# Kernel optimization log

Measured on AMD Instinct MI355X. Metric: run time of the kernel, lower is better.

The kernel has to match this reference:

```python
import math
import jax, jax.numpy as jnp
import numpy as np

B, S, D, H, HD, FF = 2, 2048, 2048, 16, 128, 5632
EPS = 1e-5


def rmsnorm(h, w):
    # LLaMA RMSNorm: x * rsqrt(mean(x^2) + eps) * weight
    return h * jax.lax.rsqrt(jnp.mean(h * h, axis=-1, keepdims=True) + EPS) * w


def cross_attn(q_in, kv_in, wq, wk, wv, wo):
    # start_pos = 0 and zero-init cache => keys/values are exactly the fresh xk/xv
    b, sq, _ = q_in.shape
    sk = kv_in.shape[1]
    q = (q_in @ wq.T).reshape(b, sq, H, HD)
    k = (kv_in @ wk.T).reshape(b, sk, H, HD)
    v = (kv_in @ wv.T).reshape(b, sk, H, HD)
    scores = jnp.einsum('bqhd,bkhd->bhqk', q, k) / math.sqrt(HD)
    p = jax.nn.softmax(scores.astype(jnp.float32), axis=-1).astype(q.dtype)
    o = jnp.einsum('bhqk,bkhd->bqhd', p, v).reshape(b, sq, H * HD)
    return o @ wo.T


def llama_output(h, residual_in, w1, w2, w3, norm_w):
    # SwiGLU FFN then post-residual RMSNorm (as in LLaMAOutput)
    ff = (jax.nn.silu(h @ w1.T) * (h @ w3.T)) @ w2.T
    return rmsnorm(ff + residual_in, norm_w)


def setup_inputs() -> dict:
    key = jax.random.key(0)
    ks = jax.random.split(key, 20)
    w = lambda k, shape: jax.random.normal(k, shape, jnp.float32) * 0.02
    return {
        'x': jax.random.normal(ks[0], (B, S, D), jnp.float32),
        'y': jax.random.normal(ks[1], (B, S, D), jnp.float32),
        'attn_norm_w': jnp.ones((D,), jnp.float32),
        'wq_x': w(ks[2], (D, D)), 'wk_x': w(ks[3], (D, D)),
        'wv_x': w(ks[4], (D, D)), 'wo_x': w(ks[5], (D, D)),
        'wq_y': w(ks[6], (D, D)), 'wk_y': w(ks[7], (D, D)),
        'wv_y': w(ks[8], (D, D)), 'wo_y': w(ks[9], (D, D)),
        'w1_x': w(ks[10], (FF, D)), 'w2_x': w(ks[11], (D, FF)), 'w3_x': w(ks[12], (FF, D)),
        'ffn_norm_x': jnp.ones((D,), jnp.float32),
        'w1_y': w(ks[13], (FF, D)), 'w2_y': w(ks[14], (D, FF)), 'w3_y': w(ks[15], (FF, D)),
        'ffn_norm_y': jnp.ones((D,), jnp.float32),
        'start_pos': 0,
    }


def reference(x, y, attn_norm_w,
              wq_x, wk_x, wv_x, wo_x,
              wq_y, wk_y, wv_y, wo_y,
              w1_x, w2_x, w3_x, ffn_norm_x,
              w1_y, w2_y, w3_y, ffn_norm_y,
              start_pos):
    del start_pos  # 0: cache slice [:, :0+S] equals fresh xk/xv
    xn = rmsnorm(x, attn_norm_w)
    yn = rmsnorm(y, attn_norm_w)
    out_x = cross_attn(xn, yn, wq_x, wk_x, wv_x, wo_x)
    out_y = cross_attn(yn, xn, wq_y, wk_y, wv_y, wo_y)
    return (llama_output(out_x, x, w1_x, w2_x, w3_x, ffn_norm_x),
            llama_output(out_y, y, w1_y, w2_y, w3_y, ffn_norm_y))
```

## Files before the change

### kernel.cpp

```cpp
#include <hip/hip_runtime.h>
#include <cstdio>
#include <cstdint>
#include <cstddef>

#define B_ 2
#define S_ 2048
#define D_ 2048
#define H_ 16
#define HD_ 128
#define FF_ 5632

typedef unsigned short u16;
typedef float f32x4 __attribute__((ext_vector_type(4)));
typedef __bf16 bf16x8 __attribute__((ext_vector_type(8)));
typedef short s16x8 __attribute__((ext_vector_type(8)));
typedef short s16x4 __attribute__((ext_vector_type(4)));

__device__ __forceinline__ u16 f2bf(float f) {
  unsigned u = __builtin_bit_cast(unsigned, f);
  u += 0x7fffu + ((u >> 16) & 1u);
  return (u16)(u >> 16);
}
__device__ __forceinline__ float bf2f(u16 h) {
  unsigned u = ((unsigned)h) << 16;
  return __builtin_bit_cast(float, u);
}

__device__ __forceinline__ void async_ld16(const void* g, void* l) {
  __builtin_amdgcn_global_load_lds(
      (__attribute__((address_space(1))) void*)(unsigned long long)g,
      (__attribute__((address_space(3))) void*)(unsigned)(unsigned long long)l,
      16, 0, 0);
}

__global__ __launch_bounds__(256) void k_cvt_bf16(
    const float* __restrict__ in, u16* __restrict__ out, int n8) {
  const int i = blockIdx.x * 256 + threadIdx.x;
  if (i >= n8) return;
  const float4* p = (const float4*)in + (size_t)i * 2;
  const float4 a = p[0], b = p[1];
  s16x8 o;
  o[0] = (short)f2bf(a.x); o[1] = (short)f2bf(a.y);
  o[2] = (short)f2bf(a.z); o[3] = (short)f2bf(a.w);
  o[4] = (short)f2bf(b.x); o[5] = (short)f2bf(b.y);
  o[6] = (short)f2bf(b.z); o[7] = (short)f2bf(b.w);
  *(s16x8*)(out + (size_t)i * 8) = o;
}

__global__ __launch_bounds__(256) void k_rmsnorm_bf16(
    const float* __restrict__ x, const float* __restrict__ w, u16* __restrict__ out) {
  const int row = blockIdx.x;
  const int t = threadIdx.x;
  const float* xr = x + (size_t)row * D_;
  const float4 a = ((const float4*)xr)[t];
  const float4 b = ((const float4*)xr)[t + 256];
  float ss = a.x * a.x + a.y * a.y + a.z * a.z + a.w * a.w +
             b.x * b.x + b.y * b.y + b.z * b.z + b.w * b.w;
#pragma unroll
  for (int off = 1; off < 64; off <<= 1) ss += __shfl_xor(ss, off);
  __shared__ float red[4];
  if ((t & 63) == 0) red[t >> 6] = ss;
  __syncthreads();
  const float scale =
      rsqrtf((red[0] + red[1] + red[2] + red[3]) * (1.0f / (float)D_) + 1e-5f);
  const float4 wa = ((const float4*)w)[t];
  const float4 wb = ((const float4*)w)[t + 256];
  u16* orow = out + (size_t)row * D_;
  s16x4 o0, o1;
  o0[0] = (short)f2bf(a.x * scale * wa.x);
  o0[1] = (short)f2bf(a.y * scale * wa.y);
  o0[2] = (short)f2bf(a.z * scale * wa.z);
  o0[3] = (short)f2bf(a.w * scale * wa.w);
  o1[0] = (short)f2bf(b.x * scale * wb.x);
  o1[1] = (short)f2bf(b.y * scale * wb.y);
  o1[2] = (short)f2bf(b.z * scale * wb.z);
  o1[3] = (short)f2bf(b.w * scale * wb.w);
  *(s16x4*)(orow + t * 4) = o0;
  *(s16x4*)(orow + (t + 256) * 4) = o1;
}

__global__ __launch_bounds__(256) void k_add_rmsnorm(
    const float* __restrict__ ff, const float* __restrict__ res,
    const float* __restrict__ w, float* __restrict__ out) {
  const int row = blockIdx.x;
  const int t = threadIdx.x;
  const float4 fa = ((const float4*)(ff + (size_t)row * D_))[t];
  const float4 fb = ((const float4*)(ff + (size_t)row * D_))[t + 256];
  const float4 ra = ((const float4*)(res + (size_t)row * D_))[t];
  const float4 rb = ((const float4*)(res + (size_t)row * D_))[t + 256];
  float4 ha, hb2;
  ha.x = fa.x + ra.x; ha.y = fa.y + ra.y; ha.z = fa.z + ra.z; ha.w = fa.w + ra.w;
  hb2.x = fb.x + rb.x; hb2.y = fb.y + rb.y; hb2.z = fb.z + rb.z; hb2.w = fb.w + rb.w;
  float ss = ha.x * ha.x + ha.y * ha.y + ha.z * ha.z + ha.w * ha.w +
             hb2.x * hb2.x + hb2.y * hb2.y + hb2.z * hb2.z + hb2.w * hb2.w;
#pragma unroll
  for (int off = 1; off < 64; off <<= 1) ss += __shfl_xor(ss, off);
  __shared__ float red[4];
  if ((t & 63) == 0) red[t >> 6] = ss;
  __syncthreads();
  const float scale =
      rsqrtf((red[0] + red[1] + red[2] + red[3]) * (1.0f / (float)D_) + 1e-5f);
  const float4 wa = ((const float4*)w)[t];
  const float4 wb = ((const float4*)w)[t + 256];
  float4 o0, o1;
  o0.x = ha.x * scale * wa.x; o0.y = ha.y * scale * wa.y;
  o0.z = ha.z * scale * wa.z; o0.w = ha.w * scale * wa.w;
  o1.x = hb2.x * scale * wb.x; o1.y = hb2.y * scale * wb.y;
  o1.z = hb2.z * scale * wb.z; o1.w = hb2.w * scale * wb.w;
  float* orow = out + (size_t)row * D_;
  ((float4*)orow)[t] = o0;
  ((float4*)orow)[t + 256] = o1;
}

__global__ __launch_bounds__(256) void k_silu_mul(
    const u16* __restrict__ gcat, u16* __restrict__ out) {
  const int idx = blockIdx.x * 256 + threadIdx.x;
  const int row = idx / 704;
  const int c = (idx - row * 704) * 8;
  const s16x8 gv = *(const s16x8*)(gcat + (size_t)row * 11264 + c);
  const s16x8 uv = *(const s16x8*)(gcat + (size_t)row * 11264 + 5632 + c);
  s16x8 ov;
#pragma unroll
  for (int j = 0; j < 8; j++) {
    float gf = bf2f((u16)gv[j]);
    float uf = bf2f((u16)uv[j]);
    float s = gf / (1.0f + __expf(-gf));
    ov[j] = (short)f2bf(s * uf);
  }
  *(s16x8*)(out + (size_t)row * 5632 + c) = ov;
}

template <int MODE>
__global__ __launch_bounds__(256, 2) void k_gemm_bt(
    const u16* __restrict__ A, const u16* __restrict__ Bm, void* __restrict__ Cp,
    u16* __restrict__ VT, int M, int N, int K, int ldc) {
  __shared__ __align__(16) u16 sA[128 * 32];
  __shared__ __align__(16) u16 sB[128 * 32];
  const int tid = threadIdx.x;
  const int lane = tid & 63;
  const int wave = tid >> 6;
  const int l15 = lane & 15;
  const int quad = lane >> 4;
  const int wm = (wave >> 1) * 64;
  const int wn = (wave & 1) * 64;
  const int bm = blockIdx.y * 128;
  const int bn = blockIdx.x * 128;

  const int sr = tid >> 2;
  const int sc = (tid & 3) * 8;
  const u16* pa = A + (size_t)(bm + sr) * K + sc;
  const u16* pb = Bm + (size_t)(bn + sr) * K + sc;
  u16* la = &sA[tid * 8];
  u16* lb = &sB[tid * 8];
  const size_t half = (size_t)64 * K;

  f32x4 acc[4][4] = {};
  const u16* ra = &sA[(wm + l15) * 32 + quad * 8];
  const u16* rb = &sB[(wn + l15) * 32 + quad * 8];

  for (int k0 = 0; k0 < K; k0 += 32) {
    async_ld16(pa, la);
    async_ld16(pa + half, la + 2048);
    async_ld16(pb, lb);
    async_ld16(pb + half, lb + 2048);
    pa += 32;
    pb += 32;
    __syncthreads();
    bf16x8 af[4], bfr[4];
#pragma unroll
    for (int i = 0; i < 4; i++) af[i] = *(const bf16x8*)(ra + i * 512);
#pragma unroll
    for (int j = 0; j < 4; j++) bfr[j] = *(const bf16x8*)(rb + j * 512);
#pragma unroll
    for (int i = 0; i < 4; i++)
#pragma unroll
      for (int j = 0; j < 4; j++)
        acc[i][j] = __builtin_amdgcn_mfma_f32_16x16x32_bf16(af[i], bfr[j],
                                                            acc[i][j], 0, 0, 0);
    __syncthreads();
  }

  if (MODE == 2 && bn >= 4096) {
#pragma unroll
    for (int i = 0; i < 4; i++)
#pragma unroll
      for (int j = 0; j < 4; j++) {
        const int row0 = bm + wm + i * 16 + quad * 4;
        const int cv = bn + wn + j * 16 + l15 - 4096;
        s16x4 o;
#pragma unroll
        for (int r = 0; r < 4; r++) o[r] = (short)f2bf(acc[i][j][r]);
        *(s16x4*)(VT + (size_t)cv * 4096 + row0) = o;
      }
    return;
  }
#pragma unroll
  for (int i = 0; i < 4; i++)
#pragma unroll
    for (int j = 0; j < 4; j++) {
      const int row0 = bm + wm + i * 16 + quad * 4;
      const int col = bn + wn + j * 16 + l15;
      if (MODE == 1) {
        float* C = (float*)Cp;
#pragma unroll
        for (int r = 0; r < 4; r++)
          C[(size_t)(row0 + r) * ldc + col] = acc[i][j][r];
      } else {
        u16* C = (u16*)Cp;
#pragma unroll
        for (int r = 0; r < 4; r++)
          C[(size_t)(row0 + r) * ldc + col] = f2bf(acc[i][j][r]);
      }
    }
}

__global__ __launch_bounds__(256) void k_flash(
    const u16* __restrict__ Qm, const u16* __restrict__ Km,
    const u16* __restrict__ VTm, u16* __restrict__ Om) {
  __shared__ __align__(16) u16 sK[32 * 136];
  __shared__ __align__(16) u16 sVT[128 * 40];
  __shared__ __align__(16) u16 sP[4][32 * 40];

  const int tid = threadIdx.x;
  const int lane = tid & 63;
  const int wave = tid >> 6;
  const int l15 = lane & 15;
  const int quad = lane >> 4;

  const int b = blockIdx.z;
  const int h = blockIdx.y;
  const int q0 = blockIdx.x * 128;
  const int LDQ = 6144;
  const size_t rowbase = (size_t)b * 2048;

  bf16x8 aq[2][4];
#pragma unroll
  for (int mi = 0; mi < 2; mi++) {
    const u16* qp = Qm + (rowbase + q0 + wave * 32 + mi * 16 + l15) * LDQ + h * 128;
#pragma unroll
    for (int c = 0; c < 4; c++)
      aq[mi][c] = *(const bf16x8*)(qp + c * 32 + quad * 8);
  }

  f32x4 o[2][8] = {};
  float l[2][4] = {};

  const int kr0 = tid >> 4;
  const int kc = (tid & 15) * 8;
  const int vhd = tid >> 2;
  const int vko = (tid & 3) * 8;

  const u16* Kbase = Km + rowbase * LDQ + h * 128;
  const u16* Vbase = VTm + (size_t)(h * 128) * 4096 + rowbase;

  const float rs = 0.08838834764831845f;

  for (int k0 = 0; k0 < S_; k0 += 32) {
    __syncthreads();
    {
      const s16x8 kv0 = *(const s16x8*)(Kbase + (size_t)(k0 + kr0) * LDQ + kc);
      const s16x8 kv1 = *(const s16x8*)(Kbase + (size_t)(k0 + kr0 + 16) * LDQ + kc);
      const s16x8 vv0 = *(const s16x8*)(Vbase + (size_t)vhd * 4096 + k0 + vko);
      const s16x8 vv1 = *(const s16x8*)(Vbase + (size_t)(vhd + 64) * 4096 + k0 + vko);
      *(s16x8*)(&sK[kr0 * 136 + kc]) = kv0;
      *(s16x8*)(&sK[(kr0 + 16) * 136 + kc]) = kv1;
      *(s16x8*)(&sVT[vhd * 40 + vko]) = vv0;
      *(s16x8*)(&sVT[(vhd + 64) * 40 + vko]) = vv1;
    }
    __syncthreads();

    bf16x8 bk[2][4];
#pragma unroll
    for (int nt = 0; nt < 2; nt++)
#pragma unroll
      for (int c = 0; c < 4; c++)
        bk[nt][c] = *(const bf16x8*)(&sK[(nt * 16 + l15) * 136 + c * 32 + quad * 8]);

#pragma unroll
    for (int mi = 0; mi < 2; mi++) {
      f32x4 s[2] = {};
#pragma unroll
      for (int nt = 0; nt < 2; nt++)
#pragma unroll
        for (int c = 0; c < 4; c++)
          s[nt] = __builtin_amdgcn_mfma_f32_16x16x32_bf16(aq[mi][c], bk[nt][c],
                                                          s[nt], 0, 0, 0);
#pragma unroll
      for (int nt = 0; nt < 2; nt++)
#pragma unroll
        for (int r = 0; r < 4; r++) {
          float pv = __expf(s[nt][r] * rs);
          l[mi][r] += pv;
          sP[wave][(mi * 16 + quad * 4 + r) * 40 + nt * 16 + l15] = f2bf(pv);
        }
    }

    bf16x8 ap[2];
#pragma unroll
    for (int mi = 0; mi < 2; mi++)
      ap[mi] = *(const bf16x8*)(&sP[wave][(mi * 16 + l15) * 40 + quad * 8]);
#pragma unroll
    for (int ht = 0; ht < 8; ht++) {
      bf16x8 bv = *(const bf16x8*)(&sVT[(ht * 16 + l15) * 40 + quad * 8]);
#pragma unroll
      for (int mi = 0; mi < 2; mi++)
        o[mi][ht] = __builtin_amdgcn_mfma_f32_16x16x32_bf16(ap[mi], bv,
                                                            o[mi][ht], 0, 0, 0);
    }
  }

#pragma unroll
  for (int mi = 0; mi < 2; mi++)
#pragma unroll
    for (int r = 0; r < 4; r++) {
      float s = l[mi][r];
      s += __shfl_xor(s, 1);
      s += __shfl_xor(s, 2);
      s += __shfl_xor(s, 4);
      s += __shfl_xor(s, 8);
      l[mi][r] = 1.0f / s;
    }
#pragma unroll
  for (int mi = 0; mi < 2; mi++)
#pragma unroll
    for (int r = 0; r < 4; r++) {
      const size_t ro =
          (rowbase + q0 + wave * 32 + mi * 16 + quad * 4 + r) * (size_t)D_ +
          (size_t)h * HD_;
      const float inv = l[mi][r];
#pragma unroll
      for (int ht = 0; ht < 8; ht++)
        Om[ro + ht * 16 + l15] = f2bf(o[mi][ht][r] * inv);
    }
}

extern "C" void kernel_launch(void* const* d_in, const int* in_sizes, int n_in,
                              void* d_out, int out_size, void* d_ws, size_t ws_size,
                              hipStream_t stream) {
  (void)in_sizes; (void)n_in; (void)out_size;

  const float* x = (const float*)d_in[0];
  const float* y = (const float*)d_in[1];
  const float* attn_norm_w = (const float*)d_in[2];
  const float* wq[2] = {(const float*)d_in[3], (const float*)d_in[7]};
  const float* wk[2] = {(const float*)d_in[4], (const float*)d_in[8]};
  const float* wv[2] = {(const float*)d_in[5], (const float*)d_in[9]};
  const float* wo[2] = {(const float*)d_in[6], (const float*)d_in[10]};
  const float* w1[2] = {(const float*)d_in[11], (const float*)d_in[15]};
  const float* w2[2] = {(const float*)d_in[12], (const float*)d_in[16]};
  const float* w3[2] = {(const float*)d_in[13], (const float*)d_in[17]};
  const float* fnw[2] = {(const float*)d_in[14], (const float*)d_in[18]};

  char* ws = (char*)d_ws;
  const size_t A0 = 0;
  const size_t A1 = 16777216;
  const size_t W_ = 33554432;
  const size_t Q1 = 79691776;
  const size_t Q2 = 130023424;
  const size_t V1 = 180355072;
  const size_t V2 = 197132288;
  const size_t GB = 213909504;
  const size_t NEED = 260046848;
  if (ws_size < NEED) {
    fprintf(stderr, "kernel_launch: ws too small: %zu < %zu\n", ws_size, NEED);
    return;
  }
  u16* xn = (u16*)(ws + A0);
  u16* yn = (u16*)(ws + A1);
  u16* wslot = (u16*)(ws + W_);
  u16* qkvA = (u16*)(ws + Q1);
  u16* qkvB = (u16*)(ws + Q2);
  u16* vtA = (u16*)(ws + V1);
  u16* vtB = (u16*)(ws + V2);
  u16* ao = (u16*)(ws + A0);
  u16* hbx = (u16*)(ws + A1);
  u16* hby = (u16*)(ws + V1);
  u16* gcat = (u16*)(ws + Q1);
  u16* gbuf = (u16*)(ws + GB);
  float* ff = (float*)(ws + Q1);

  const size_t WOFF = (size_t)2048 * 2048;

  k_rmsnorm_bf16<<<4096, 256, 0, stream>>>(x, attn_norm_w, xn);
  k_rmsnorm_bf16<<<4096, 256, 0, stream>>>(y, attn_norm_w, yn);

  const dim3 gqkv(48, 32);
  const dim3 gproj(16, 32);
  const dim3 gw13(88, 32);

  k_cvt_bf16<<<2048, 256, 0, stream>>>(wq[0], wslot, 524288);
  k_cvt_bf16<<<2048, 256, 0, stream>>>(wk[1], wslot + WOFF, 524288);
  k_cvt_bf16<<<2048, 256, 0, stream>>>(wv[1], wslot + 2 * WOFF, 524288);
  k_gemm_bt<2><<<gqkv, 256, 0, stream>>>(xn, wslot, qkvA, vtA, 4096, 6144, 2048, 6144);
  k_cvt_bf16<<<2048, 256, 0, stream>>>(wq[1], wslot, 524288);
  k_cvt_bf16<<<2048, 256, 0, stream>>>(wk[0], wslot + WOFF, 524288);
  k_cvt_bf16<<<2048, 256, 0, stream>>>(wv[0], wslot + 2 * WOFF, 524288);
  k_gemm_bt<2><<<gqkv, 256, 0, stream>>>(yn, wslot, qkvB, vtB, 4096, 6144, 2048, 6144);

  k_flash<<<dim3(16, 16, 2), 256, 0, stream>>>(qkvA, qkvB + 2048, vtB, ao);
  k_cvt_bf16<<<2048, 256, 0, stream>>>(wo[0], wslot, 524288);
  k_gemm_bt<0><<<gproj, 256, 0, stream>>>(ao, wslot, hbx, nullptr, 4096, 2048, 2048, 2048);

  k_flash<<<dim3(16, 16, 2), 256, 0, stream>>>(qkvB, qkvA + 2048, vtA, ao);
  k_cvt_bf16<<<2048, 256, 0, stream>>>(wo[1], wslot, 524288);
  k_gemm_bt<0><<<gproj, 256, 0, stream>>>(ao, wslot, hby, nullptr, 4096, 2048, 2048, 2048);

  const float* resid[2] = {x, y};
  float* outp[2] = {(float*)d_out, (float*)d_out + (size_t)8388608};
  u16* hb[2] = {hbx, hby};
  const size_t W13OFF = (size_t)FF_ * 2048;

  for (int s = 0; s < 2; s++) {
    k_cvt_bf16<<<5632, 256, 0, stream>>>(w1[s], wslot, 1441792);
    k_cvt_bf16<<<5632, 256, 0, stream>>>(w3[s], wslot + W13OFF, 1441792);
    k_gemm_bt<0><<<gw13, 256, 0, stream>>>(hb[s], wslot, gcat, nullptr, 4096, 11264, 2048, 11264);
    k_silu_mul<<<11264, 256, 0, stream>>>(gcat, gbuf);
    k_cvt_bf16<<<5632, 256, 0, stream>>>(w2[s], wslot, 1441792);
    k_gemm_bt<1><<<gproj, 256, 0, stream>>>(gbuf, wslot, ff, nullptr, 4096, 2048, 5632, 2048);
    k_add_rmsnorm<<<4096, 256, 0, stream>>>(ff, resid[s], fnw[s], outp[s]);
  }
}
```

Before: 1.772 ms.

## Add 256x256 double-buffered GEMM kernel for QKV and W1/W3 projections

Result: faster. 1.685 ms (-4.9%).

```diff
diff --git a/kernel.cpp b/kernel.cpp
--- a/kernel.cpp
+++ b/kernel.cpp
@@ -180,20 +180,6 @@
     __syncthreads();
   }
 
-  if (MODE == 2 && bn >= 4096) {
-#pragma unroll
-    for (int i = 0; i < 4; i++)
-#pragma unroll
-      for (int j = 0; j < 4; j++) {
-        const int row0 = bm + wm + i * 16 + quad * 4;
-        const int cv = bn + wn + j * 16 + l15 - 4096;
-        s16x4 o;
-#pragma unroll
-        for (int r = 0; r < 4; r++) o[r] = (short)f2bf(acc[i][j][r]);
-        *(s16x4*)(VT + (size_t)cv * 4096 + row0) = o;
-      }
-    return;
-  }
 #pragma unroll
   for (int i = 0; i < 4; i++)
 #pragma unroll
@@ -211,6 +197,119 @@
         for (int r = 0; r < 4; r++)
           C[(size_t)(row0 + r) * ldc + col] = f2bf(acc[i][j][r]);
       }
+    }
+  (void)VT;
+}
+
+template <int MODE>
+__global__ __launch_bounds__(512, 2) void k_gemm256(
+    const u16* __restrict__ A, const u16* __restrict__ Bm, void* __restrict__ Cp,
+    u16* __restrict__ VT, int M, int N, int K, int ldc) {
+  __shared__ __align__(16) char smem[131072];
+  (void)M; (void)N;
+  const int tid = threadIdx.x;
+  const int lane = tid & 63;
+  const int w = tid >> 6;
+  const int l15 = lane & 15;
+  const int quad = lane >> 4;
+  const int wr = w >> 2;
+  const int wc = w & 3;
+  const int bm = blockIdx.y * 256;
+  const int bn = blockIdx.x * 256;
+
+  const int srow = w * 8 + (lane >> 3);
+  const int scol = ((lane & 7) ^ ((lane >> 3) & 7)) * 8;
+  const int sloff = w * 1024 + lane * 16;
+  const u16* const pa = A + (size_t)(bm + srow) * K + scol;
+  const u16* const pb = Bm + (size_t)(bn + srow) * K + scol;
+  const size_t rs64 = (size_t)64 * K;
+
+  const int fxor = (l15 & 7) << 4;
+  const int c0 = (quad * 16) ^ fxor;
+  const int c1 = (64 + quad * 16) ^ fxor;
+  const int aRow = (wr * 128 + l15) * 128;
+  const int bRow = 32768 + (wc * 64 + l15) * 128;
+
+  f32x4 acc[8][4] = {};
+  const int NT = K >> 6;
+
+  auto stage = [&](int ph, int buf, int kt) {
+    const int isB = ph >> 1;
+    const int h = ph & 1;
+    const u16* g = (isB ? pb : pa) + (size_t)(h * 128) * K + kt * 64;
+    char* l0 = smem + buf * 65536 + isB * 32768 + h * 16384 + sloff;
+    async_ld16(g, l0);
+    async_ld16(g + rs64, l0 + 8192);
+  };
+
+#pragma unroll
+  for (int ph = 0; ph < 4; ph++) stage(ph, 0, 0);
+
+  for (int t = 0; t < NT; t++) {
+    const char* base = smem + (t & 1) * 65536;
+    bf16x8 bfr[2][4];
+#pragma unroll
+    for (int q = 0; q < 4; q++) {
+      const bool pf = (t + 1 < NT);
+      if (pf) stage(q, (t & 1) ^ 1, t + 1);
+      if (q == 0) {
+        if (pf) { asm volatile("s_waitcnt vmcnt(2)" ::: "memory"); }
+        else    { asm volatile("s_waitcnt vmcnt(0)" ::: "memory"); }
+        __builtin_amdgcn_s_barrier();
+        asm volatile("" ::: "memory");
+#pragma unroll
+        for (int ni = 0; ni < 4; ni++) {
+          bfr[0][ni] = *(const bf16x8*)(base + bRow + ni * 2048 + c0);
+          bfr[1][ni] = *(const bf16x8*)(base + bRow + ni * 2048 + c1);
+        }
+      }
+      bf16x8 af[2][2];
+#pragma unroll
+      for (int dm = 0; dm < 2; dm++) {
+        af[dm][0] = *(const bf16x8*)(base + aRow + (2 * q + dm) * 2048 + c0);
+        af[dm][1] = *(const bf16x8*)(base + aRow + (2 * q + dm) * 2048 + c1);
+      }
+      __builtin_amdgcn_s_setprio(1);
+#pragma unroll
+      for (int dm = 0; dm < 2; dm++)
+#pragma unroll
+        for (int ni = 0; ni < 4; ni++) {
+          acc[2 * q + dm][ni] = __builtin_amdgcn_mfma_f32_16x16x32_bf16(
+              af[dm][0], bfr[0][ni], acc[2 * q + dm][ni], 0, 0, 0);
+          acc[2 * q + dm][ni] = __builtin_amdgcn_mfma_f32_16x16x32_bf16(
+              af[dm][1], bfr[1][ni], acc[2 * q + dm][ni], 0, 0, 0);
+        }
+      __builtin_amdgcn_s_setprio(0);
+      asm volatile("" ::: "memory");
+      __builtin_amdgcn_s_barrier();
+      asm volatile("" ::: "memory");
+    }
+  }
+
+  if (MODE == 2 && bn >= 4096) {
+#pragma unroll
+    for (int mi = 0; mi < 8; mi++)
+#pragma unroll
+      for (int ni = 0; ni < 4; ni++) {
+        const int row0 = bm + wr * 128 + mi * 16 + quad * 4;
+        const int cv = bn + wc * 64 + ni * 16 + l15 - 4096;
+        s16x4 o;
+#pragma unroll
+        for (int r = 0; r < 4; r++) o[r] = (short)f2bf(acc[mi][ni][r]);
+        *(s16x4*)(VT + (size_t)cv * 4096 + row0) = o;
+      }
+    return;
+  }
+  u16* C = (u16*)Cp;
+#pragma unroll
+  for (int mi = 0; mi < 8; mi++)
+#pragma unroll
+    for (int ni = 0; ni < 4; ni++) {
+      const int row0 = bm + wr * 128 + mi * 16 + quad * 4;
+      const int col = bn + wc * 64 + ni * 16 + l15;
+#pragma unroll
+      for (int r = 0; r < 4; r++)
+        C[(size_t)(row0 + r) * ldc + col] = f2bf(acc[mi][ni][r]);
     }
 }
 
@@ -384,18 +483,18 @@
   k_rmsnorm_bf16<<<4096, 256, 0, stream>>>(x, attn_norm_w, xn);
   k_rmsnorm_bf16<<<4096, 256, 0, stream>>>(y, attn_norm_w, yn);
 
-  const dim3 gqkv(48, 32);
+  const dim3 gqkv(24, 16);
   const dim3 gproj(16, 32);
-  const dim3 gw13(88, 32);
+  const dim3 gw13(44, 16);
 
   k_cvt_bf16<<<2048, 256, 0, stream>>>(wq[0], wslot, 524288);
   k_cvt_bf16<<<2048, 256, 0, stream>>>(wk[1], wslot + WOFF, 524288);
   k_cvt_bf16<<<2048, 256, 0, stream>>>(wv[1], wslot + 2 * WOFF, 524288);
-  k_gemm_bt<2><<<gqkv, 256, 0, stream>>>(xn, wslot, qkvA, vtA, 4096, 6144, 2048, 6144);
+  k_gemm256<2><<<gqkv, 512, 0, stream>>>(xn, wslot, qkvA, vtA, 4096, 6144, 2048, 6144);
   k_cvt_bf16<<<2048, 256, 0, stream>>>(wq[1], wslot, 524288);
   k_cvt_bf16<<<2048, 256, 0, stream>>>(wk[0], wslot + WOFF, 524288);
   k_cvt_bf16<<<2048, 256, 0, stream>>>(wv[0], wslot + 2 * WOFF, 524288);
-  k_gemm_bt<2><<<gqkv, 256, 0, stream>>>(yn, wslot, qkvB, vtB, 4096, 6144, 2048, 6144);
+  k_gemm256<2><<<gqkv, 512, 0, stream>>>(yn, wslot, qkvB, vtB, 4096, 6144, 2048, 6144);
 
   k_flash<<<dim3(16, 16, 2), 256, 0, stream>>>(qkvA, qkvB + 2048, vtB, ao);
   k_cvt_bf16<<<2048, 256, 0, stream>>>(wo[0], wslot, 524288);
@@ -413,7 +512,7 @@
   for (int s = 0; s < 2; s++) {
     k_cvt_bf16<<<5632, 256, 0, stream>>>(w1[s], wslot, 1441792);
     k_cvt_bf16<<<5632, 256, 0, stream>>>(w3[s], wslot + W13OFF, 1441792);
-    k_gemm_bt<0><<<gw13, 256, 0, stream>>>(hb[s], wslot, gcat, nullptr, 4096, 11264, 2048, 11264);
+    k_gemm256<0><<<gw13, 512, 0, stream>>>(hb[s], wslot, gcat, nullptr, 4096, 11264, 2048, 11264);
     k_silu_mul<<<11264, 256, 0, stream>>>(gcat, gbuf);
     k_cvt_bf16<<<5632, 256, 0, stream>>>(w2[s], wslot, 1441792);
     k_gemm_bt<1><<<gproj, 256, 0, stream>>>(gbuf, wslot, ff, nullptr, 4096, 2048, 5632, 2048);
```

## Replace GEMM with 256x128 triple-buffered swizzled LDS pipeline kernel

Applied to the files above, without the earlier changes.

Result: faster. 1.600 ms (-9.7%).

```diff
diff --git a/kernel.cpp b/kernel.cpp
--- a/kernel.cpp
+++ b/kernel.cpp
@@ -131,85 +131,147 @@
 }
 
 template <int MODE>
-__global__ __launch_bounds__(256, 2) void k_gemm_bt(
+__global__ __launch_bounds__(512, 2) void k_gemmR(
     const u16* __restrict__ A, const u16* __restrict__ Bm, void* __restrict__ Cp,
-    u16* __restrict__ VT, int M, int N, int K, int ldc) {
-  __shared__ __align__(16) u16 sA[128 * 32];
-  __shared__ __align__(16) u16 sB[128 * 32];
+    u16* __restrict__ VT, int K, int ldc) {
+  __shared__ __align__(16) char smem[147456];
   const int tid = threadIdx.x;
   const int lane = tid & 63;
-  const int wave = tid >> 6;
+  const int w = tid >> 6;
   const int l15 = lane & 15;
   const int quad = lane >> 4;
-  const int wm = (wave >> 1) * 64;
-  const int wn = (wave & 1) * 64;
-  const int bm = blockIdx.y * 128;
-  const int bn = blockIdx.x * 128;
-
-  const int sr = tid >> 2;
-  const int sc = (tid & 3) * 8;
-  const u16* pa = A + (size_t)(bm + sr) * K + sc;
-  const u16* pb = Bm + (size_t)(bn + sr) * K + sc;
-  u16* la = &sA[tid * 8];
-  u16* lb = &sB[tid * 8];
-  const size_t half = (size_t)64 * K;
+  const int wr = w >> 1;
+  const int wc = w & 1;
+
+  const int gx = gridDim.x;
+  const int nwg = gx * gridDim.y;
+  const int flat = blockIdx.y * gx + blockIdx.x;
+  const int swz = (flat & 7) * (nwg >> 3) + (flat >> 3);
+  const int bm = (swz / gx) * 256;
+  const int bn = (swz % gx) * 128;
+
+  const int srow = tid >> 3;
+  const int scol = ((tid & 7) ^ ((tid >> 3) & 7)) * 8;
+  const int sloff = tid * 16;
+  const u16* const pa = A + (size_t)(bm + srow) * K + scol;
+  const u16* const pb = Bm + (size_t)(bn + srow) * K + scol;
+
+  auto stage = [&](int u, int kt, int ring) {
+    char* base = smem + ring;
+    if (u < 4)
+      async_ld16(pa + (size_t)(u * 64) * K + kt * 64, base + u * 8192 + sloff);
+    else
+      async_ld16(pb + (size_t)((u - 4) * 64) * K + kt * 64,
+                 base + 32768 + (u - 4) * 8192 + sloff);
+  };
+
+  const int fxor = (l15 & 7) << 4;
+  const int c0 = (quad * 16) ^ fxor;
+  const int c1 = (64 + quad * 16) ^ fxor;
+  const int aRow = (wr * 64 + l15) * 128;
+  const int bRow = 32768 + (wc * 64 + l15) * 128;
 
   f32x4 acc[4][4] = {};
-  const u16* ra = &sA[(wm + l15) * 32 + quad * 8];
-  const u16* rb = &sB[(wn + l15) * 32 + quad * 8];
-
-  for (int k0 = 0; k0 < K; k0 += 32) {
-    async_ld16(pa, la);
-    async_ld16(pa + half, la + 2048);
-    async_ld16(pb, lb);
-    async_ld16(pb + half, lb + 2048);
-    pa += 32;
-    pb += 32;
-    __syncthreads();
-    bf16x8 af[4], bfr[4];
-#pragma unroll
-    for (int i = 0; i < 4; i++) af[i] = *(const bf16x8*)(ra + i * 512);
-#pragma unroll
-    for (int j = 0; j < 4; j++) bfr[j] = *(const bf16x8*)(rb + j * 512);
-#pragma unroll
-    for (int i = 0; i < 4; i++)
-#pragma unroll
-      for (int j = 0; j < 4; j++)
-        acc[i][j] = __builtin_amdgcn_mfma_f32_16x16x32_bf16(af[i], bfr[j],
-                                                            acc[i][j], 0, 0, 0);
-    __syncthreads();
+  const int NT = K >> 6;
+
+#pragma unroll
+  for (int u = 0; u < 6; u++) stage(u, 0, 0);
+#pragma unroll
+  for (int u = 0; u < 6; u++) stage(u, 1, 49152);
+
+  int rcur = 0, rnext = 49152, rstage = 98304;
+
+  for (int t = 0; t < NT; t++) {
+    if (t + 1 < NT) { asm volatile("s_waitcnt vmcnt(6)" ::: "memory"); }
+    else            { asm volatile("s_waitcnt vmcnt(0)" ::: "memory"); }
+    __builtin_amdgcn_s_barrier();
+    asm volatile("" ::: "memory");
+
+    const char* cb = smem + rcur;
+    const bool pf = (t + 2 < NT);
+
+    if (pf) { stage(0, t + 2, rstage); stage(1, t + 2, rstage); stage(2, t + 2, rstage); }
+    bf16x8 bfr[2][4];
+#pragma unroll
+    for (int ni = 0; ni < 4; ni++) {
+      bfr[0][ni] = *(const bf16x8*)(cb + bRow + ni * 2048 + c0);
+      bfr[1][ni] = *(const bf16x8*)(cb + bRow + ni * 2048 + c1);
+    }
+    {
+      bf16x8 af[2][2];
+#pragma unroll
+      for (int dm = 0; dm < 2; dm++) {
+        af[dm][0] = *(const bf16x8*)(cb + aRow + dm * 2048 + c0);
+        af[dm][1] = *(const bf16x8*)(cb + aRow + dm * 2048 + c1);
+      }
+      __builtin_amdgcn_s_setprio(1);
+#pragma unroll
+      for (int dm = 0; dm < 2; dm++)
+#pragma unroll
+        for (int ni = 0; ni < 4; ni++) {
+          acc[dm][ni] = __builtin_amdgcn_mfma_f32_16x16x32_bf16(
+              af[dm][0], bfr[0][ni], acc[dm][ni], 0, 0, 0);
+          acc[dm][ni] = __builtin_amdgcn_mfma_f32_16x16x32_bf16(
+              af[dm][1], bfr[1][ni], acc[dm][ni], 0, 0, 0);
+        }
+      __builtin_amdgcn_s_setprio(0);
+    }
+
+    if (pf) { stage(3, t + 2, rstage); stage(4, t + 2, rstage); stage(5, t + 2, rstage); }
+    {
+      bf16x8 af[2][2];
+#pragma unroll
+      for (int dm = 0; dm < 2; dm++) {
+        af[dm][0] = *(const bf16x8*)(cb + aRow + (2 + dm) * 2048 + c0);
+        af[dm][1] = *(const bf16x8*)(cb + aRow + (2 + dm) * 2048 + c1);
+      }
+      __builtin_amdgcn_s_setprio(1);
+#pragma unroll
+      for (int dm = 0; dm < 2; dm++)
+#pragma unroll
+        for (int ni = 0; ni < 4; ni++) {
+          acc[2 + dm][ni] = __builtin_amdgcn_mfma_f32_16x16x32_bf16(
+              af[dm][0], bfr[0][ni], acc[2 + dm][ni], 0, 0, 0);
+          acc[2 + dm][ni] = __builtin_amdgcn_mfma_f32_16x16x32_bf16(
+              af[dm][1], bfr[1][ni], acc[2 + dm][ni], 0, 0, 0);
+        }
+      __builtin_amdgcn_s_setprio(0);
+    }
+    asm volatile("" ::: "memory");
+
+    const int tmp = rcur; rcur = rnext; rnext = rstage; rstage = tmp;
   }
 
   if (MODE == 2 && bn >= 4096) {
 #pragma unroll
-    for (int i = 0; i < 4; i++)
-#pragma unroll
-      for (int j = 0; j < 4; j++) {
-        const int row0 = bm + wm + i * 16 + quad * 4;
-        const int cv = bn + wn + j * 16 + l15 - 4096;
+    for (int mi = 0; mi < 4; mi++)
+#pragma unroll
+      for (int ni = 0; ni < 4; ni++) {
+        const int row0 = bm + wr * 64 + mi * 16 + quad * 4;
+        const int cv = bn + wc * 64 + ni * 16 + l15 - 4096;
         s16x4 o;
 #pragma unroll
-        for (int r = 0; r < 4; r++) o[r] = (short)f2bf(acc[i][j][r]);
+        for (int r = 0; r < 4; r++) o[r] = (short)f2bf(acc[mi][ni][r]);
         *(s16x4*)(VT + (size_t)cv * 4096 + row0) = o;
       }
     return;
   }
 #pragma unroll
-  for (int i = 0; i < 4; i++)
-#pragma unroll
-    for (int j = 0; j < 4; j++) {
-      const int row0 = bm + wm + i * 16 + quad * 4;
-      const int col = bn + wn + j * 16 + l15;
+  for (int mi = 0; mi < 4; mi++)
+#pragma unroll
+    for (int ni = 0; ni < 4; ni++) {
+      const int row0 = bm + wr * 64 + mi * 16 + quad * 4;
+      const int col = bn + wc * 64 + ni * 16 + l15;
       if (MODE == 1) {
         float* C = (float*)Cp;
 #pragma unroll
         for (int r = 0; r < 4; r++)
-          C[(size_t)(row0 + r) * ldc + col] = acc[i][j][r];
+          C[(size_t)(row0 + r) * ldc + col] = acc[mi][ni][r];
       } else {
         u16* C = (u16*)Cp;
 #pragma unroll
         for (int r = 0; r < 4; r++)
-          C[(size_t)(row0 + r) * ldc + col] = f2bf(acc[i][j][r]);
+          C[(size_t)(row0 + r) * ldc + col] = f2bf(acc[mi][ni][r]);
       }
     }
 }
@@ -384,26 +446,26 @@
   k_rmsnorm_bf16<<<4096, 256, 0, stream>>>(x, attn_norm_w, xn);
   k_rmsnorm_bf16<<<4096, 256, 0, stream>>>(y, attn_norm_w, yn);
 
-  const dim3 gqkv(48, 32);
-  const dim3 gproj(16, 32);
-  const dim3 gw13(88, 32);
+  const dim3 gqkv(48, 16);
+  const dim3 gproj(16, 16);
+  const dim3 gw13(88, 16);
 
   k_cvt_bf16<<<2048, 256, 0, stream>>>(wq[0], wslot, 524288);
   k_cvt_bf16<<<2048, 256, 0, stream>>>(wk[1], wslot + WOFF, 524288);
   k_cvt_bf16<<<2048, 256, 0, stream>>>(wv[1], wslot + 2 * WOFF, 524288);
-  k_gemm_bt<2><<<gqkv, 256, 0, stream>>>(xn, wslot, qkvA, vtA, 4096, 6144, 2048, 6144);
+  k_gemmR<2><<<gqkv, 512, 0, stream>>>(xn, wslot, qkvA, vtA, 2048, 6144);
   k_cvt_bf16<<<2048, 256, 0, stream>>>(wq[1], wslot, 524288);
   k_cvt_bf16<<<2048, 256, 0, stream>>>(wk[0], wslot + WOFF, 524288);
   k_cvt_bf16<<<2048, 256, 0, stream>>>(wv[0], wslot + 2 * WOFF, 524288);
-  k_gemm_bt<2><<<gqkv, 256, 0, stream>>>(yn, wslot, qkvB, vtB, 4096, 6144, 2048, 6144);
+  k_gemmR<2><<<gqkv, 512, 0, stream>>>(yn, wslot, qkvB, vtB, 2048, 6144);
 
   k_flash<<<dim3(16, 16, 2), 256, 0, stream>>>(qkvA, qkvB + 2048, vtB, ao);
   k_cvt_bf16<<<2048, 256, 0, stream>>>(wo[0], wslot, 524288);
-  k_gemm_bt<0><<<gproj, 256, 0, stream>>>(ao, wslot, hbx, nullptr, 4096, 2048, 2048, 2048);
+  k_gemmR<0><<<gproj, 512, 0, stream>>>(ao, wslot, hbx, nullptr, 2048, 2048);
 
   k_flash<<<dim3(16, 16, 2), 256, 0, stream>>>(qkvB, qkvA + 2048, vtA, ao);
   k_cvt_bf16<<<2048, 256, 0, stream>>>(wo[1], wslot, 524288);
-  k_gemm_bt<0><<<gproj, 256, 0, stream>>>(ao, wslot, hby, nullptr, 4096, 2048, 2048, 2048);
+  k_gemmR<0><<<gproj, 512, 0, stream>>>(ao, wslot, hby, nullptr, 2048, 2048);
 
   const float* resid[2] = {x, y};
   float* outp[2] = {(float*)d_out, (float*)d_out + (size_t)8388608};
@@ -413,10 +475,10 @@
   for (int s = 0; s < 2; s++) {
     k_cvt_bf16<<<5632, 256, 0, stream>>>(w1[s], wslot, 1441792);
     k_cvt_bf16<<<5632, 256, 0, stream>>>(w3[s], wslot + W13OFF, 1441792);
-    k_gemm_bt<0><<<gw13, 256, 0, stream>>>(hb[s], wslot, gcat, nullptr, 4096, 11264, 2048, 11264);
+    k_gemmR<0><<<gw13, 512, 0, stream>>>(hb[s], wslot, gcat, nullptr, 2048, 11264);
     k_silu_mul<<<11264, 256, 0, stream>>>(gcat, gbuf);
     k_cvt_bf16<<<5632, 256, 0, stream>>>(w2[s], wslot, 1441792);
-    k_gemm_bt<1><<<gproj, 256, 0, stream>>>(gbuf, wslot, ff, nullptr, 4096, 2048, 5632, 2048);
+    k_gemmR<1><<<gproj, 512, 0, stream>>>(gbuf, wslot, ff, nullptr, 5632, 2048);
     k_add_rmsnorm<<<4096, 256, 0, stream>>>(ff, resid[s], fnw[s], outp[s]);
   }
 }
```
